# Optimization experiments

Measured on AMD Instinct MI355X. Metric: run time of the kernel, lower is better.

The kernel has to match this reference:

```python
import jax, jax.numpy as jnp
import numpy as np

N = 4096
E = 262144
IN_C = 128
OUT_C = 128
EDGE_D = 16


def setup_inputs() -> dict:
    key = jax.random.key(0)
    k = jax.random.split(key, 8)
    x = jax.random.normal(k[0], (N, IN_C), dtype=jnp.float32)
    edge_index = jax.random.randint(k[1], (2, E), 0, N, dtype=jnp.int64)
    edge_attr = jax.random.normal(k[2], (N, N, EDGE_D), dtype=jnp.float32)
    # nn.Linear params: y = x @ W.T + b; store pre-transposed W for x @ W
    s1 = 1.0 / np.sqrt(IN_C + EDGE_D)
    s2 = 1.0 / np.sqrt(OUT_C)
    W1 = jax.random.uniform(k[3], (IN_C + EDGE_D, OUT_C), jnp.float32, -s1, s1)
    b1 = jax.random.uniform(k[4], (OUT_C,), jnp.float32, -s1, s1)
    W2 = jax.random.uniform(k[5], (OUT_C, OUT_C), jnp.float32, -s2, s2)
    b2 = jax.random.uniform(k[6], (OUT_C,), jnp.float32, -s2, s2)
    return {"x": x, "edge_index": edge_index, "edge_attr": edge_attr,
            "W1": W1, "b1": b1, "W2": W2, "b2": b2}


def reference(x, edge_index, edge_attr, W1, b1, W2, b2):
    row, col = edge_index[0], edge_index[1]
    x_row = x[row]                      # [E, IN_C] gather
    e = edge_attr[row, col]             # [E, EDGE_D] gather from dense NxN table
    h = jnp.concatenate([x_row, e], axis=-1)     # [E, IN_C+EDGE_D]
    h = jax.nn.relu(h @ W1 + b1)                  # [E, OUT_C]
    h = jax.nn.relu(h @ W2 + b2)                  # [E, OUT_C]
    # global_add_pool(out, col): scatter-add edges into node buckets by col
    return jax.ops.segment_sum(h, col, num_segments=x.shape[0])  # [N, OUT_C]
```

## Files before the change

### kernel.cpp

```cpp
#include <hip/hip_runtime.h>
#include <hip/hip_bf16.h>

#define NN 4096
#define IC 128
#define OC 128
#define ED 16
#define EPB 64
#define NT 256
#define NSLOT 8
#define NBLK 512
#define NCPY 8

typedef __bf16 bf16x8 __attribute__((ext_vector_type(8)));
typedef float  f32x16 __attribute__((ext_vector_type(16)));

#define BAR() do { asm volatile("s_waitcnt lgkmcnt(0)" ::: "memory"); \
    __builtin_amdgcn_s_barrier(); \
    __builtin_amdgcn_sched_barrier(0); } while (0)

__device__ __forceinline__ unsigned short bf16u(float f) {
    unsigned int u = __float_as_uint(f);
    u = (u + 0x7FFFu + ((u >> 16) & 1u)) >> 16;
    return (unsigned short)u;
}
__device__ __forceinline__ float bf16tof(unsigned short h) {
    return __uint_as_float(((unsigned int)h) << 16);
}
__device__ __forceinline__ int swzk(int row) { return (row ^ (row >> 3)) & 7; }

__global__ __launch_bounds__(128) void k_xw1(
    const float* __restrict__ x, const float* __restrict__ W1,
    const float* __restrict__ b1, const int* __restrict__ eidx,
    float* __restrict__ xw1b, float* __restrict__ out,
    int* __restrict__ hist8, int E)
{
    __shared__ float xs[8][IC];
    const int t = threadIdx.x;
    const int r0 = blockIdx.x * 8;
    #pragma unroll
    for (int r = 0; r < 8; ++r) xs[r][t] = x[(size_t)(r0 + r) * IC + t];

    const float4 z = make_float4(0.f, 0.f, 0.f, 0.f);
    float4* o4 = (float4*)out;
    o4[blockIdx.x * 256 + t]       = z;
    o4[blockIdx.x * 256 + 128 + t] = z;

    {
        const int e0 = blockIdx.x * 512;
        #pragma unroll
        for (int j = 0; j < 4; ++j) {
            const int k = (2 * blockIdx.x + (j >> 1)) & (NCPY - 1);
            atomicAdd(&hist8[k * 4096 + eidx[E + e0 + t + j * 128]], 1);
        }
    }

    __syncthreads();
    float acc[8];
    const float bb = b1[t];
    #pragma unroll
    for (int r = 0; r < 8; ++r) acc[r] = bb;
    #pragma unroll 4
    for (int k = 0; k < IC; ++k) {
        const float w = W1[(size_t)k * OC + t];
        #pragma unroll
        for (int r = 0; r < 8; ++r) acc[r] = fmaf(xs[r][k], w, acc[r]);
    }
    #pragma unroll
    for (int r = 0; r < 8; ++r) xw1b[(size_t)(r0 + r) * OC + t] = acc[r];
}

__global__ __launch_bounds__(256) void k_scan(
    const int* __restrict__ hist8, int* __restrict__ cursor8)
{
    __shared__ int tot[256];
    __shared__ int base[256];
    const int t = threadIdx.x;
    int loc[16];
    int s = 0;
    #pragma unroll
    for (int j = 0; j < 16; ++j) {
        const int b = t * 16 + j;
        int sb = 0;
        #pragma unroll
        for (int k = 0; k < NCPY; ++k) sb += hist8[k * 4096 + b];
        loc[j] = s; s += sb;
    }
    tot[t] = s;
    __syncthreads();
    if (t == 0) {
        int a = 0;
        for (int i = 0; i < 256; ++i) { base[i] = a; a += tot[i]; }
    }
    __syncthreads();
    const int a = base[t];
    #pragma unroll
    for (int j = 0; j < 16; ++j) {
        const int b = t * 16 + j;
        int off = a + loc[j];
        #pragma unroll
        for (int k = 0; k < NCPY; ++k) {
            cursor8[k * 4096 + b] = off;
            off += hist8[k * 4096 + b];
        }
    }
}

__global__ void k_scatter(const int* __restrict__ eidx, int* __restrict__ cursor8,
                          int2* __restrict__ csr, int E) {
    const int i = blockIdx.x * blockDim.x + threadIdx.x;
    const int k = blockIdx.x & (NCPY - 1);
    if (i < E) {
        const int row = eidx[i];
        const int col = eidx[E + i];
        const int pos = atomicAdd(&cursor8[k * 4096 + col], 1);
        csr[pos] = make_int2(row, col);
    }
}

__global__ __launch_bounds__(NT, 2) void k_edge8(
    const int2* __restrict__ csr, const float* __restrict__ eattr,
    const float* __restrict__ xw1b, const float* __restrict__ W1,
    const float* __restrict__ W2, const float* __restrict__ b2,
    float* __restrict__ out, int E)
{
    extern __shared__ char smem[];
    char*   const h1hi = smem;
    char*   const h1lo = smem + 16384;
    float4* const eaL  = (float4*)(smem + 32768);
    float4* const w1L  = (float4*)(smem + 36864);
    float*  const lacc = (float*)(smem + 45056);
    int*    const srowL = (int*)(smem + 49152);
    int*    const scolL = srowL + 128;

    const int t   = threadIdx.x;
    const int l   = t & 63;
    const int wid = t >> 6;
    const int cg  = t & 15, eg = t >> 4;
    const int c0  = cg << 3, e0 = eg << 2;
    const int sz  = (eg >> 1) & 3;
    const int em  = t >> 2, q = t & 3;
    const int esz = (em >> 3) & 3;

    const int lm  = l & 31;
    const int hi  = l >> 5;
    const int c2  = wid * 32 + lm;

    w1L[t]       = ((const float4*)(W1 + (size_t)IC * OC))[t];
    w1L[t + NT]  = ((const float4*)(W1 + (size_t)IC * OC))[t + NT];

    bf16x8 w2h[8], w2l[8];
    #pragma unroll
    for (int s = 0; s < 8; ++s) {
        union { unsigned short us[8]; bf16x8 v; } Uh, Ul;
        #pragma unroll
        for (int j = 0; j < 8; ++j) {
            const float w = W2[(size_t)(s * 16 + hi * 8 + j) * OC + c2];
            const unsigned short h = bf16u(w);
            Uh.us[j] = h;
            Ul.us[j] = bf16u(w - bf16tof(h));
        }
        w2h[s] = Uh.v; w2l[s] = Ul.v;
    }
    const float b2s = b2[c2];

    #pragma unroll
    for (int i = 0; i < 4; ++i) lacc[t + NT * i] = 0.f;

    const int nper = (E / EPB) / NBLK;
    const int ibb  = blockIdx.x * nper;

    if (t < EPB) {
        const int2 rc = csr[(size_t)ibb * EPB + t];
        srowL[t] = rc.x;
        scolL[t] = rc.y;
    }
    __syncthreads();

    float4 pA;
    {
        const int r = srowL[em], c = scolL[em];
        pA = ((const float4*)(eattr + ((size_t)r * NN + c) * ED))[q];
    }
    int2 pidx;
    {
        const int ibn = (nper > 1) ? 1 : 0;
        pidx = (t < EPB) ? csr[(size_t)(ibb + ibn) * EPB + t] : make_int2(0, 0);
    }

    int cur = 0;
    for (int ii = 0; ii < nper; ++ii) {
        const int nxt = cur ^ 1;

        BAR();

        if (t < EPB) { srowL[nxt * EPB + t] = pidx.x; scolL[nxt * EPB + t] = pidx.y; }
        eaL[(em * 4 + q) ^ esz] = pA;
        float4 xa[4], xb[4];
        #pragma unroll
        for (int ri = 0; ri < 4; ++ri) {
            const int row = srowL[cur * EPB + e0 + ri];
            const float4* p = (const float4*)(xw1b + (size_t)row * OC + c0);
            xa[ri] = p[0]; xb[ri] = p[1];
        }
        BAR();

        float4 ha[4], hb[4];
        #pragma unroll
        for (int ri = 0; ri < 4; ++ri) { ha[ri] = xa[ri]; hb[ri] = xb[ri]; }
        #pragma unroll
        for (int dc = 0; dc < 4; ++dc) {
            float4 ev[4];
            #pragma unroll
            for (int ri = 0; ri < 4; ++ri)
                ev[ri] = eaL[((e0 + ri) * 4 + dc) ^ sz];
            #pragma unroll
            for (int dd = 0; dd < 4; ++dd) {
                const int d = dc * 4 + dd;
                const float4 wA = w1L[d * 32 + cg * 2];
                const float4 wB = w1L[d * 32 + cg * 2 + 1];
                #pragma unroll
                for (int ri = 0; ri < 4; ++ri) {
                    const float evd = (dd == 0) ? ev[ri].x : (dd == 1) ? ev[ri].y
                                     : (dd == 2) ? ev[ri].z : ev[ri].w;
                    ha[ri].x = fmaf(evd, wA.x, ha[ri].x);
                    ha[ri].y = fmaf(evd, wA.y, ha[ri].y);
                    ha[ri].z = fmaf(evd, wA.z, ha[ri].z);
                    ha[ri].w = fmaf(evd, wA.w, ha[ri].w);
                    hb[ri].x = fmaf(evd, wB.x, hb[ri].x);
                    hb[ri].y = fmaf(evd, wB.y, hb[ri].y);
                    hb[ri].z = fmaf(evd, wB.z, hb[ri].z);
                    hb[ri].w = fmaf(evd, wB.w, hb[ri].w);
                }
            }
        }
        #pragma unroll
        for (int ri = 0; ri < 4; ++ri) {
            const int row = e0 + ri;
            float v[8] = { ha[ri].x, ha[ri].y, ha[ri].z, ha[ri].w,
                           hb[ri].x, hb[ri].y, hb[ri].z, hb[ri].w };
            union { unsigned short us[8]; uint4 qv; } Hh, Hl;
            #pragma unroll
            for (int j = 0; j < 8; ++j) {
                const float f = fmaxf(v[j], 0.f);
                const unsigned short h = bf16u(f);
                Hh.us[j] = h;
                Hl.us[j] = bf16u(f - bf16tof(h));
            }
            const int boff = (cg * 16) ^ (swzk(row) << 4);
            *(uint4*)(h1hi + row * 256 + boff) = Hh.qv;
            *(uint4*)(h1lo + row * 256 + boff) = Hl.qv;
        }
        {
            const int r = srowL[nxt * EPB + em], c = scolL[nxt * EPB + em];
            pA = ((const float4*)(eattr + ((size_t)r * NN + c) * ED))[q];
        }
        {
            const int iin = (ii + 2 < nper) ? (ii + 2) : (nper - 1);
            pidx = (t < EPB) ? csr[(size_t)(ibb + iin) * EPB + t] : make_int2(0, 0);
        }
        BAR();

        f32x16 acc0 = (f32x16)(0.0f);
        f32x16 acc1 = (f32x16)(0.0f);
        const int arow0 = lm;
        const int arow1 = 32 + lm;
        const int ak0 = swzk(arow0) << 4;
        const int ak1 = swzk(arow1) << 4;
        #pragma unroll
        for (int s = 0; s < 8; ++s) {
            const int kb = s * 32 + hi * 16;
            const bf16x8 aH0 = *(const bf16x8*)(h1hi + arow0 * 256 + (kb ^ ak0));
            const bf16x8 aL0 = *(const bf16x8*)(h1lo + arow0 * 256 + (kb ^ ak0));
            const bf16x8 aH1 = *(const bf16x8*)(h1hi + arow1 * 256 + (kb ^ ak1));
            const bf16x8 aL1 = *(const bf16x8*)(h1lo + arow1 * 256 + (kb ^ ak1));
            acc0 = __builtin_amdgcn_mfma_f32_32x32x16_bf16(aH0, w2h[s], acc0, 0, 0, 0);
            acc1 = __builtin_amdgcn_mfma_f32_32x32x16_bf16(aH1, w2h[s], acc1, 0, 0, 0);
            acc0 = __builtin_amdgcn_mfma_f32_32x32x16_bf16(aL0, w2h[s], acc0, 0, 0, 0);
            acc1 = __builtin_amdgcn_mfma_f32_32x32x16_bf16(aL1, w2h[s], acc1, 0, 0, 0);
            acc0 = __builtin_amdgcn_mfma_f32_32x32x16_bf16(aH0, w2l[s], acc0, 0, 0, 0);
            acc1 = __builtin_amdgcn_mfma_f32_32x32x16_bf16(aH1, w2l[s], acc1, 0, 0, 0);
        }

        const int colbase = scolL[cur * EPB];
        #pragma unroll
        for (int p = 0; p < 2; ++p) {
            const int mbase = p * 32 + 4 * hi;
            #pragma unroll
            for (int g = 0; g < 4; ++g) {
                const int eb = mbase + 8 * g;
                float sv;
                {
                    const float a0 = (p == 0) ? acc0[4 * g] : acc1[4 * g];
                    sv = fmaxf(a0 + b2s, 0.f);
                }
                int ccur = scolL[cur * EPB + eb];
                #pragma unroll
                for (int j = 1; j < 4; ++j) {
                    const float aj = (p == 0) ? acc0[4 * g + j] : acc1[4 * g + j];
                    const float v = fmaxf(aj + b2s, 0.f);
                    const int c = scolL[cur * EPB + eb + j];
                    if (c == ccur) {
                        sv += v;
                    } else {
                        const int slot = ccur - colbase;
                        if (slot < NSLOT) {
                            if (sv != 0.f) atomicAdd(&lacc[slot * OC + c2], sv);
                        } else {
                            if (sv != 0.f) atomicAdd(&out[(size_t)ccur * OC + c2], sv);
                        }
                        ccur = c; sv = v;
                    }
                }
                const int slot = ccur - colbase;
                if (slot < NSLOT) {
                    if (sv != 0.f) atomicAdd(&lacc[slot * OC + c2], sv);
                } else {
                    if (sv != 0.f) atomicAdd(&out[(size_t)ccur * OC + c2], sv);
                }
            }
        }
        BAR();

        int span = scolL[cur * EPB + EPB - 1] - colbase + 1;
        if (span > NSLOT) span = NSLOT;
        for (int idx = t; idx < span * OC; idx += NT) {
            const float v = lacc[idx];
            lacc[idx] = 0.f;
            if (v != 0.f)
                atomicAdd(&out[(size_t)(colbase + (idx >> 7)) * OC + (idx & 127)], v);
        }
        cur = nxt;
    }
}

#define LDS_BYTES 50176

extern "C" void kernel_launch(void* const* d_in, const int* in_sizes, int n_in,
                              void* d_out, int out_size, void* d_ws, size_t ws_size,
                              hipStream_t stream) {
    const float* x    = (const float*)d_in[0];
    const int*   eidx = (const int*)d_in[1];
    const float* ea   = (const float*)d_in[2];
    const float* W1   = (const float*)d_in[3];
    const float* b1   = (const float*)d_in[4];
    const float* W2   = (const float*)d_in[5];
    const float* b2   = (const float*)d_in[6];
    float* out = (float*)d_out;

    const int E = in_sizes[1] / 2;

    char* ws = (char*)d_ws;
    float* xw1b    = (float*)ws;
    int*   hist8   = (int*)(ws + 2097152);
    int*   cursor8 = (int*)(ws + 2097152 + 131072);
    int2*  csr     = (int2*)(ws + 2097152 + 262144);

    hipMemsetAsync(hist8, 0, 131072, stream);
    k_xw1<<<NN / 8, 128, 0, stream>>>(x, W1, b1, eidx, xw1b, out, hist8, E);
    k_scan<<<1, 256, 0, stream>>>(hist8, cursor8);
    k_scatter<<<(E + 255) / 256, 256, 0, stream>>>(eidx, cursor8, csr, E);

    hipFuncSetAttribute(reinterpret_cast<const void*>(k_edge8),
                        hipFuncAttributeMaxDynamicSharedMemorySize, LDS_BYTES);
    k_edge8<<<NBLK, NT, LDS_BYTES, stream>>>(csr, ea, xw1b, W1, W2, b2, out, E);
}
```

Baseline: 140.9 us.

## Deepen edge-kernel software pipeline and drop one barrier per tile

Restructures the per-tile loop of the edge kernel. Index slots become a 4-deep ring and the edge-attribute staging buffer is double-buffered. The next tile's xw1b rows and edge attributes are prefetched into registers during the current tile, and the edge attributes are written to the alternate LDS buffer before the existing barrier. This removes the two barriers at the top of each iteration and hides global gather latency behind the MFMA and scatter phases. In exchange it uses more LDS (about 55 KB per block) and more live registers, which may pressure occupancy at 2 blocks per CU.

```diff
diff --git a/kernel.cpp b/kernel.cpp
--- a/kernel.cpp
+++ b/kernel.cpp
@@ -117,7 +117,7 @@
     }
 }
 
-__global__ __launch_bounds__(NT, 2) void k_edge8(
+__global__ __launch_bounds__(NT, 2) void k_edge9(
     const int2* __restrict__ csr, const float* __restrict__ eattr,
     const float* __restrict__ xw1b, const float* __restrict__ W1,
     const float* __restrict__ W2, const float* __restrict__ b2,
@@ -127,10 +127,10 @@
     char*   const h1hi = smem;
     char*   const h1lo = smem + 16384;
     float4* const eaL  = (float4*)(smem + 32768);
-    float4* const w1L  = (float4*)(smem + 36864);
-    float*  const lacc = (float*)(smem + 45056);
-    int*    const srowL = (int*)(smem + 49152);
-    int*    const scolL = srowL + 128;
+    float4* const w1L  = (float4*)(smem + 40960);
+    float*  const lacc = (float*)(smem + 49152);
+    int*    const srowL = (int*)(smem + 53248);
+    int*    const scolL = srowL + 256;
 
     const int t   = threadIdx.x;
     const int l   = t & 63;
@@ -170,9 +170,11 @@
     const int ibb  = blockIdx.x * nper;
 
     if (t < EPB) {
-        const int2 rc = csr[(size_t)ibb * EPB + t];
-        srowL[t] = rc.x;
-        scolL[t] = rc.y;
+        const int2 r0v = csr[(size_t)ibb * EPB + t];
+        srowL[t] = r0v.x; scolL[t] = r0v.y;
+        const int ib1 = (nper > 1) ? 1 : 0;
+        const int2 r1v = csr[(size_t)(ibb + ib1) * EPB + t];
+        srowL[64 + t] = r1v.x; scolL[64 + t] = r1v.y;
     }
     __syncthreads();
 
@@ -181,28 +183,24 @@
         const int r = srowL[em], c = scolL[em];
         pA = ((const float4*)(eattr + ((size_t)r * NN + c) * ED))[q];
     }
+    eaL[(em * 4 + q) ^ esz] = pA;
+    float4 xa[4], xb[4];
+    #pragma unroll
+    for (int ri = 0; ri < 4; ++ri) {
+        const int row = srowL[e0 + ri];
+        const float4* p = (const float4*)(xw1b + (size_t)row * OC + c0);
+        xa[ri] = p[0]; xb[ri] = p[1];
+    }
     int2 pidx;
     {
-        const int ibn = (nper > 1) ? 1 : 0;
-        pidx = (t < EPB) ? csr[(size_t)(ibb + ibn) * EPB + t] : make_int2(0, 0);
-    }
-
-    int cur = 0;
+        const int ib2 = (nper > 2) ? 2 : (nper - 1);
+        pidx = (t < EPB) ? csr[(size_t)(ibb + ib2) * EPB + t] : make_int2(0, 0);
+    }
+    __syncthreads();
+
     for (int ii = 0; ii < nper; ++ii) {
-        const int nxt = cur ^ 1;
-
-        BAR();
-
-        if (t < EPB) { srowL[nxt * EPB + t] = pidx.x; scolL[nxt * EPB + t] = pidx.y; }
-        eaL[(em * 4 + q) ^ esz] = pA;
-        float4 xa[4], xb[4];
-        #pragma unroll
-        for (int ri = 0; ri < 4; ++ri) {
-            const int row = srowL[cur * EPB + e0 + ri];
-            const float4* p = (const float4*)(xw1b + (size_t)row * OC + c0);
-            xa[ri] = p[0]; xb[ri] = p[1];
-        }
-        BAR();
+        const int cb  = ii & 1;
+        const int ib4 = ii & 3;
 
         float4 ha[4], hb[4];
         #pragma unroll
@@ -212,7 +210,7 @@
             float4 ev[4];
             #pragma unroll
             for (int ri = 0; ri < 4; ++ri)
-                ev[ri] = eaL[((e0 + ri) * 4 + dc) ^ sz];
+                ev[ri] = eaL[cb * 256 + ((((e0 + ri) * 4 + dc)) ^ sz)];
             #pragma unroll
             for (int dd = 0; dd < 4; ++dd) {
                 const int d = dc * 4 + dd;
@@ -250,12 +248,23 @@
             *(uint4*)(h1hi + row * 256 + boff) = Hh.qv;
             *(uint4*)(h1lo + row * 256 + boff) = Hl.qv;
         }
+        if (t < EPB) {
+            srowL[((ii + 2) & 3) * 64 + t] = pidx.x;
+            scolL[((ii + 2) & 3) * 64 + t] = pidx.y;
+        }
         {
-            const int r = srowL[nxt * EPB + em], c = scolL[nxt * EPB + em];
+            const int jn = (ii + 1) & 3;
+            const int r = srowL[jn * 64 + em], c = scolL[jn * 64 + em];
             pA = ((const float4*)(eattr + ((size_t)r * NN + c) * ED))[q];
+            #pragma unroll
+            for (int ri = 0; ri < 4; ++ri) {
+                const int row = srowL[jn * 64 + e0 + ri];
+                const float4* p = (const float4*)(xw1b + (size_t)row * OC + c0);
+                xa[ri] = p[0]; xb[ri] = p[1];
+            }
         }
         {
-            const int iin = (ii + 2 < nper) ? (ii + 2) : (nper - 1);
+            const int iin = (ii + 3 < nper) ? (ii + 3) : (nper - 1);
             pidx = (t < EPB) ? csr[(size_t)(ibb + iin) * EPB + t] : make_int2(0, 0);
         }
         BAR();
@@ -281,7 +290,7 @@
             acc1 = __builtin_amdgcn_mfma_f32_32x32x16_bf16(aH1, w2l[s], acc1, 0, 0, 0);
         }
 
-        const int colbase = scolL[cur * EPB];
+        const int colbase = scolL[ib4 * 64];
         #pragma unroll
         for (int p = 0; p < 2; ++p) {
             const int mbase = p * 32 + 4 * hi;
@@ -293,12 +302,12 @@
                     const float a0 = (p == 0) ? acc0[4 * g] : acc1[4 * g];
                     sv = fmaxf(a0 + b2s, 0.f);
                 }
-                int ccur = scolL[cur * EPB + eb];
+                int ccur = scolL[ib4 * 64 + eb];
                 #pragma unroll
                 for (int j = 1; j < 4; ++j) {
                     const float aj = (p == 0) ? acc0[4 * g + j] : acc1[4 * g + j];
                     const float v = fmaxf(aj + b2s, 0.f);
-                    const int c = scolL[cur * EPB + eb + j];
+                    const int c = scolL[ib4 * 64 + eb + j];
                     if (c == ccur) {
                         sv += v;
                     } else {
@@ -319,9 +328,10 @@
                 }
             }
         }
+        eaL[(cb ^ 1) * 256 + ((em * 4 + q) ^ esz)] = pA;
         BAR();
 
-        int span = scolL[cur * EPB + EPB - 1] - colbase + 1;
+        int span = scolL[ib4 * 64 + EPB - 1] - colbase + 1;
         if (span > NSLOT) span = NSLOT;
         for (int idx = t; idx < span * OC; idx += NT) {
             const float v = lacc[idx];
@@ -329,11 +339,10 @@
             if (v != 0.f)
                 atomicAdd(&out[(size_t)(colbase + (idx >> 7)) * OC + (idx & 127)], v);
         }
-        cur = nxt;
-    }
-}
-
-#define LDS_BYTES 50176
+    }
+}
+
+#define LDS_BYTES 55296
 
 extern "C" void kernel_launch(void* const* d_in, const int* in_sizes, int n_in,
                               void* d_out, int out_size, void* d_ws, size_t ws_size,
@@ -360,7 +369,7 @@
     k_scan<<<1, 256, 0, stream>>>(hist8, cursor8);
     k_scatter<<<(E + 255) / 256, 256, 0, stream>>>(eidx, cursor8, csr, E);
 
-    hipFuncSetAttribute(reinterpret_cast<const void*>(k_edge8),
+    hipFuncSetAttribute(reinterpret_cast<const void*>(k_edge9),
                         hipFuncAttributeMaxDynamicSharedMemorySize, LDS_BYTES);
-    k_edge8<<<NBLK, NT, LDS_BYTES, stream>>>(csr, ea, xw1b, W1, W2, b2, out, E);
-}
+    k_edge9<<<NBLK, NT, LDS_BYTES, stream>>>(csr, ea, xw1b, W1, W2, b2, out, E);
+}
```

New measurement: 139.1 us. Within noise of the previous version (-1.2%).
